# Kernel tuning notes

Measured on AMD Instinct MI355X. Metric: run time of the kernel, lower is better.

The kernel has to match this reference:

```python
import jax, jax.numpy as jnp
import numpy as np

D_MODEL = 768
N_LAYER = 4
VOCAB = 50257
D_STATE = 16
D_CONV = 4
D_INNER = 2 * D_MODEL
DT_RANK = 48
B, L = 1, 2048


def setup_inputs() -> dict:
    key = jax.random.key(0)
    ks = jax.random.split(key, 12)
    n = lambda k, shape, s=0.02: jax.random.normal(k, shape, dtype=jnp.float32) * s
    return {
        "idx": jax.random.randint(ks[0], (B, L), 0, VOCAB, dtype=jnp.int32),
        "targets": jax.random.randint(ks[1], (B, L), 0, VOCAB, dtype=jnp.int32),
        "embedding": n(ks[2], (VOCAB, D_MODEL)),
        "norm_w": jnp.ones((N_LAYER, D_MODEL), jnp.float32),
        "in_proj_w": n(ks[3], (N_LAYER, 2 * D_INNER, D_MODEL)),
        "conv_w": n(ks[4], (N_LAYER, D_INNER, D_CONV), 0.1),
        "conv_b": jnp.zeros((N_LAYER, D_INNER), jnp.float32),
        "x_proj_w": n(ks[5], (N_LAYER, DT_RANK + 2 * D_STATE, D_INNER)),
        "dt_proj_w": n(ks[6], (N_LAYER, D_INNER, DT_RANK), 0.1),
        # bias so softplus(dt) lands in ~[0.01, 0.1] as in the official init
        "dt_proj_b": jax.random.uniform(ks[7], (N_LAYER, D_INNER), jnp.float32, -4.6, -2.3),
        # A_log = log(1..d_state), the standard S4D-real init
        "A_log": jnp.log(jnp.broadcast_to(jnp.arange(1, D_STATE + 1, dtype=jnp.float32), (N_LAYER, D_INNER, D_STATE))),
        "D_param": jnp.ones((N_LAYER, D_INNER), jnp.float32),
        "out_proj_w": n(ks[8], (N_LAYER, D_MODEL, D_INNER)),
        "norm_f_w": jnp.ones((D_MODEL,), jnp.float32),
    }


def rmsnorm(x, w, eps=1e-5):
    return x * jax.lax.rsqrt(jnp.mean(x * x, -1, keepdims=True) + eps) * w


def causal_conv1d(x, w, b):
    # x: (B,L,d_inner); w: (d_inner, K) depthwise causal conv
    K = w.shape[-1]
    Lx = x.shape[1]
    xp = jnp.pad(x, ((0, 0), (K - 1, 0), (0, 0)))
    y = b
    for k in range(K):
        y = y + xp[:, k:k + Lx, :] * w[:, k]
    return y


def selective_scan(x, dt, A, Bm, Cm, Dp):
    # x, dt: (B,L,d_inner); A: (d_inner,d_state); Bm, Cm: (B,L,d_state)
    bsz, _, d_in = x.shape

    def step(h, inp):
        x_t, dt_t, B_t, C_t = inp  # (B,d_in),(B,d_in),(B,s),(B,s)
        h = jnp.exp(dt_t[:, :, None] * A) * h + (dt_t * x_t)[:, :, None] * B_t[:, None, :]
        return h, jnp.einsum('bds,bs->bd', h, C_t)

    h0 = jnp.zeros((bsz, d_in, A.shape[-1]), x.dtype)
    _, ys = jax.lax.scan(step, h0, (x.swapaxes(0, 1), dt.swapaxes(0, 1), Bm.swapaxes(0, 1), Cm.swapaxes(0, 1)))
    return ys.swapaxes(0, 1) + x * Dp


def mamba_block(x, in_w, cw, cb, xpw, dtw, dtb, a_log, dp, ow):
    xz = x @ in_w.T  # (B,L,2*d_inner)
    xi, z = jnp.split(xz, 2, axis=-1)
    xi = jax.nn.silu(causal_conv1d(xi, cw, cb))
    xdbl = xi @ xpw.T  # (B,L,dt_rank+2*d_state)
    dt = xdbl[..., :DT_RANK]
    Bm = xdbl[..., DT_RANK:DT_RANK + D_STATE]
    Cm = xdbl[..., DT_RANK + D_STATE:]
    dt = jax.nn.softplus(dt @ dtw.T + dtb)
    A = -jnp.exp(a_log)
    y = selective_scan(xi, dt, A, Bm, Cm, dp)
    y = y * jax.nn.silu(z)
    return y @ ow.T


def reference(idx, targets, embedding, norm_w, in_proj_w, conv_w, conv_b, x_proj_w,
              dt_proj_w, dt_proj_b, A_log, D_param, out_proj_w, norm_f_w):
    x = embedding[idx]  # (B,L,D)
    for l in range(N_LAYER):
        x = x + mamba_block(rmsnorm(x, norm_w[l]), in_proj_w[l], conv_w[l], conv_b[l],
                            x_proj_w[l], dt_proj_w[l], dt_proj_b[l], A_log[l],
                            D_param[l], out_proj_w[l])
    x = rmsnorm(x, norm_f_w)
    logits = x @ embedding.T  # tied lm head, (B,L,V)
    # cross_entropy with ignore_index=-1
    logp = jax.nn.log_softmax(logits, axis=-1)
    mask = (targets >= 0).astype(logits.dtype)
    tgt = jnp.clip(targets, 0, VOCAB - 1)
    nll = -jnp.take_along_axis(logp, tgt[..., None], axis=-1)[..., 0]
    loss = jnp.sum(nll * mask) / jnp.maximum(jnp.sum(mask), 1.0)
    return (logits, loss)
```

## Files before the change

### kernel.cpp

```cpp
#include <hip/hip_runtime.h>
#include <stdint.h>


#define D_MODEL 768
#define N_LAYER 4
#define VOCAB 50257
#define D_STATE 16
#define D_INNER 1536
#define DT_RANK 48
#define LSEQ 2048
#define TCHUNK 64
#define NCHUNK 32

#define EMB_E 39321600L
#define W1E 2359296L
#define W2E 196608L
#define W3E 98304L
#define W4E 1179648L
#define PERL (W1E + W2E + W3E + W4E)
#define TOTCVT (EMB_E + 4 * PERL)

typedef unsigned short u16;
typedef __attribute__((ext_vector_type(8))) short short8;
typedef __attribute__((ext_vector_type(4))) float f32x4;

__device__ __forceinline__ u16 f2bf(float f) {
  unsigned int x = __float_as_uint(f);
  x += 0x7fffu + ((x >> 16) & 1u);
  return (u16)(x >> 16);
}
__device__ __forceinline__ float bf2f(u16 v) {
  return __uint_as_float(((unsigned int)v) << 16);
}
__device__ __forceinline__ void gl16(const void* g, void* l) {
  __builtin_amdgcn_global_load_lds((const __attribute__((address_space(1))) void*)g,
                                   (__attribute__((address_space(3))) void*)l, 16, 0, 0);
}

__global__ void k_convert_all(const float* __restrict__ emb, const float* __restrict__ in_w,
                              const float* __restrict__ xp_w, const float* __restrict__ dt_w,
                              const float* __restrict__ out_w, u16* __restrict__ dst) {
  long i = (long)blockIdx.x * 256 + threadIdx.x;
  float v;
  if (i < EMB_E) {
    long n = i / D_MODEL, k = i % D_MODEL;
    v = (n < VOCAB) ? emb[n * D_MODEL + k] : 0.0f;
  } else {
    long j = i - EMB_E;
    int l = (int)(j / PERL);
    long m = j % PERL;
    if (m < W1E) {
      v = in_w[(long)l * W1E + m];
    } else if (m < W1E + W2E) {
      long mm = m - W1E;
      long n = mm / D_INNER, k = mm % D_INNER;
      v = (n < 80) ? xp_w[(long)l * 80 * D_INNER + n * D_INNER + k] : 0.0f;
    } else if (m < W1E + W2E + W3E) {
      long mm = m - (W1E + W2E);
      long n = mm / 64, k = mm % 64;
      v = (k < DT_RANK) ? dt_w[(long)l * D_INNER * DT_RANK + n * DT_RANK + k] : 0.0f;
    } else {
      long mm = m - (W1E + W2E + W3E);
      v = out_w[(long)l * W4E + mm];
    }
  }
  dst[i] = f2bf(v);
}

__global__ void k_embed_rms(const int* __restrict__ idx, const float* __restrict__ emb,
                            const float* __restrict__ w, float* __restrict__ x,
                            u16* __restrict__ xnb) {
  int t = blockIdx.x, tid = threadIdx.x;
  __shared__ float red[256];
  const float* src = emb + (long)idx[t] * D_MODEL;
  float g[3];
  float s = 0.0f;
#pragma unroll
  for (int q = 0; q < 3; q++) {
    g[q] = src[tid + q * 256];
    s += g[q] * g[q];
  }
  red[tid] = s; __syncthreads();
  for (int o = 128; o > 0; o >>= 1) { if (tid < o) red[tid] += red[tid + o]; __syncthreads(); }
  float scale = rsqrtf(red[0] / (float)D_MODEL + 1e-5f);
#pragma unroll
  for (int q = 0; q < 3; q++) {
    int c = tid + q * 256;
    x[(long)t * D_MODEL + c] = g[q];
    xnb[(long)t * D_MODEL + c] = f2bf(g[q] * scale * w[c]);
  }
}

__global__ void k_rms_red(const float* __restrict__ part, const float* __restrict__ w,
                          float* __restrict__ x, u16* __restrict__ xnb) {
  int t = blockIdx.x, tid = threadIdx.x;
  __shared__ float red[256];
  float g[3];
  float s = 0.0f;
#pragma unroll
  for (int q = 0; q < 3; q++) {
    int c = tid + q * 256;
    long off = (long)t * D_MODEL + c;
    float v = x[off];
#pragma unroll
    for (int p = 0; p < 4; p++) v += part[(size_t)p * LSEQ * D_MODEL + off];
    g[q] = v;
    s += v * v;
  }
  red[tid] = s; __syncthreads();
  for (int o = 128; o > 0; o >>= 1) { if (tid < o) red[tid] += red[tid + o]; __syncthreads(); }
  float scale = rsqrtf(red[0] / (float)D_MODEL + 1e-5f);
#pragma unroll
  for (int q = 0; q < 3; q++) {
    int c = tid + q * 256;
    x[(long)t * D_MODEL + c] = g[q];
    xnb[(long)t * D_MODEL + c] = f2bf(g[q] * scale * w[c]);
  }
}

template<int EPI>
__global__ __launch_bounds__(256) void k_gemm2(
    const u16* __restrict__ A, const u16* __restrict__ W, void* __restrict__ Cv,
    const float* __restrict__ bias, int N, int K, int lda, int ldb, int ldc) {
  __shared__ u16 lA[2][128 * 32];
  __shared__ u16 lB[2][128 * 32];
  const int gx = gridDim.x, gy = gridDim.y;
  int id = blockIdx.x + gx * blockIdx.y;
  int q8 = (gx * gy) >> 3;
  int v = (id & 7) * q8 + (id >> 3);
  const int bx = v / gy, by = v % gy;
  const int brow = by * 128, bcol = bx * 128;
  const int tid = threadIdx.x, wid = tid >> 6, lane = tid & 63;
  const int wm = (wid >> 1) * 64, wn = (wid & 1) * 64;
  const int fr = lane & 15, fq = lane >> 4, kh = fq * 8;
  const int srow = tid >> 2, scol = (tid & 3) * 8;
  const u16* ga0 = A + (size_t)(brow + srow) * lda + scol;
  const u16* ga1 = A + (size_t)(brow + srow + 64) * lda + scol;
  const u16* gb0 = W + (size_t)(bcol + srow) * ldb + scol;
  const u16* gb1 = W + (size_t)(bcol + srow + 64) * ldb + scol;
  const int lo = srow * 32 + scol;

  f32x4 acc[4][4];
#pragma unroll
  for (int i = 0; i < 4; i++)
#pragma unroll
    for (int j = 0; j < 4; j++)
#pragma unroll
      for (int r = 0; r < 4; r++) acc[i][j][r] = 0.0f;

  auto STAGE = [&](int k0, int b) {
    gl16(ga0 + k0, &lA[b][lo]);
    gl16(ga1 + k0, &lA[b][lo + 64 * 32]);
    gl16(gb0 + k0, &lB[b][lo]);
    gl16(gb1 + k0, &lB[b][lo + 64 * 32]);
  };

  const int nt = K / 32;
  STAGE(0, 0);
  __syncthreads();
  int cur = 0;
  for (int t = 0; t < nt; t++) {
    if (t + 1 < nt) STAGE((t + 1) * 32, cur ^ 1);
    short8 af[4], bfr[4];
#pragma unroll
    for (int i = 0; i < 4; i++) af[i] = *(const short8*)(&lA[cur][(wm + i * 16 + fr) * 32 + kh]);
#pragma unroll
    for (int j = 0; j < 4; j++) bfr[j] = *(const short8*)(&lB[cur][(wn + j * 16 + fr) * 32 + kh]);
#pragma unroll
    for (int i = 0; i < 4; i++)
#pragma unroll
      for (int j = 0; j < 4; j++)
        acc[i][j] = __builtin_amdgcn_mfma_f32_16x16x32_bf16(af[i], bfr[j], acc[i][j], 0, 0, 0);
    __syncthreads();
    cur ^= 1;
  }
#pragma unroll
  for (int i = 0; i < 4; i++)
#pragma unroll
    for (int j = 0; j < 4; j++) {
      int col = bcol + wn + j * 16 + fr;
      if (col < N) {
#pragma unroll
        for (int r = 0; r < 4; r++) {
          int row = brow + wm + i * 16 + fq * 4 + r;
          float val = acc[i][j][r];
          if (EPI == 1) {
            val += bias[col];
            val = (val > 20.0f) ? val : log1pf(__expf(val));
            ((float*)Cv)[(size_t)row * ldc + col] = val;
          } else {
            ((u16*)Cv)[(size_t)row * ldc + col] = f2bf(val);
          }
        }
      }
    }
}

__global__ __launch_bounds__(256) void k_gemm_part(
    const u16* __restrict__ A, const u16* __restrict__ W, float* __restrict__ Cp,
    int N, int Ks, int lda, int ldb, int ldc) {
  __shared__ u16 lA[2][128 * 32];
  __shared__ u16 lB[2][128 * 32];
  const int gx = gridDim.x, gy = gridDim.y;
  int id = blockIdx.x + gx * blockIdx.y;
  int q8 = (gx * gy) >> 3;
  int v = (id & 7) * q8 + (id >> 3);
  const int bx = v / gy, by = v % gy;
  const int brow = by * 128, bcol = bx * 128;
  const int koff = blockIdx.z * Ks;
  const int tid = threadIdx.x, wid = tid >> 6, lane = tid & 63;
  const int wm = (wid >> 1) * 64, wn = (wid & 1) * 64;
  const int fr = lane & 15, fq = lane >> 4, kh = fq * 8;
  const int srow = tid >> 2, scol = (tid & 3) * 8;
  const u16* ga0 = A + (size_t)(brow + srow) * lda + koff + scol;
  const u16* ga1 = A + (size_t)(brow + srow + 64) * lda + koff + scol;
  const u16* gb0 = W + (size_t)(bcol + srow) * ldb + koff + scol;
  const u16* gb1 = W + (size_t)(bcol + srow + 64) * ldb + koff + scol;
  const int lo = srow * 32 + scol;

  f32x4 acc[4][4];
#pragma unroll
  for (int i = 0; i < 4; i++)
#pragma unroll
    for (int j = 0; j < 4; j++)
#pragma unroll
      for (int r = 0; r < 4; r++) acc[i][j][r] = 0.0f;

  auto STAGE = [&](int k0, int b) {
    gl16(ga0 + k0, &lA[b][lo]);
    gl16(ga1 + k0, &lA[b][lo + 64 * 32]);
    gl16(gb0 + k0, &lB[b][lo]);
    gl16(gb1 + k0, &lB[b][lo + 64 * 32]);
  };

  const int nt = Ks / 32;
  STAGE(0, 0);
  __syncthreads();
  int cur = 0;
  for (int t = 0; t < nt; t++) {
    if (t + 1 < nt) STAGE((t + 1) * 32, cur ^ 1);
    short8 af[4], bfr[4];
#pragma unroll
    for (int i = 0; i < 4; i++) af[i] = *(const short8*)(&lA[cur][(wm + i * 16 + fr) * 32 + kh]);
#pragma unroll
    for (int j = 0; j < 4; j++) bfr[j] = *(const short8*)(&lB[cur][(wn + j * 16 + fr) * 32 + kh]);
#pragma unroll
    for (int i = 0; i < 4; i++)
#pragma unroll
      for (int j = 0; j < 4; j++)
        acc[i][j] = __builtin_amdgcn_mfma_f32_16x16x32_bf16(af[i], bfr[j], acc[i][j], 0, 0, 0);
    __syncthreads();
    cur ^= 1;
  }
  float* Cz = Cp + (size_t)blockIdx.z * LSEQ * ldc;
#pragma unroll
  for (int i = 0; i < 4; i++)
#pragma unroll
    for (int j = 0; j < 4; j++) {
      int col = bcol + wn + j * 16 + fr;
      if (col < N) {
#pragma unroll
        for (int r = 0; r < 4; r++) {
          int row = brow + wm + i * 16 + fq * 4 + r;
          Cz[(size_t)row * ldc + col] = acc[i][j][r];
        }
      }
    }
}

__global__ __launch_bounds__(256) void k_gemm_logits(
    const u16* __restrict__ A, const u16* __restrict__ W, float* __restrict__ C,
    float* __restrict__ part) {
  __shared__ u16 lA[2][128 * 32];
  __shared__ u16 lB[2][128 * 32];
  const int b = blockIdx.x;
  const int xcd = b & 7, slot = b >> 3;
  const int ct = xcd * 50 + (slot >> 4), rt = slot & 15;
  const int brow = rt * 128, bcol = ct * 128;
  const int tid = threadIdx.x, wid = tid >> 6, lane = tid & 63;
  const int wm = (wid >> 1) * 64, wn = (wid & 1) * 64;
  const int fr = lane & 15, fq = lane >> 4, kh = fq * 8;
  const int srow = tid >> 2, scol = (tid & 3) * 8;
  const u16* ga0 = A + (size_t)(brow + srow) * D_MODEL + scol;
  const u16* ga1 = A + (size_t)(brow + srow + 64) * D_MODEL + scol;
  const u16* gb0 = W + (size_t)(bcol + srow) * D_MODEL + scol;
  const u16* gb1 = W + (size_t)(bcol + srow + 64) * D_MODEL + scol;
  const int lo = srow * 32 + scol;

  f32x4 acc[4][4];
#pragma unroll
  for (int i = 0; i < 4; i++)
#pragma unroll
    for (int j = 0; j < 4; j++)
#pragma unroll
      for (int r = 0; r < 4; r++) acc[i][j][r] = 0.0f;

  auto STAGE = [&](int k0, int bb) {
    gl16(ga0 + k0, &lA[bb][lo]);
    gl16(ga1 + k0, &lA[bb][lo + 64 * 32]);
    gl16(gb0 + k0, &lB[bb][lo]);
    gl16(gb1 + k0, &lB[bb][lo + 64 * 32]);
  };

  STAGE(0, 0);
  __syncthreads();
  int cur = 0;
  for (int t = 0; t < D_MODEL / 32; t++) {
    if (t + 1 < D_MODEL / 32) STAGE((t + 1) * 32, cur ^ 1);
    short8 af[4], bfr[4];
#pragma unroll
    for (int i = 0; i < 4; i++) af[i] = *(const short8*)(&lA[cur][(wm + i * 16 + fr) * 32 + kh]);
#pragma unroll
    for (int j = 0; j < 4; j++) bfr[j] = *(const short8*)(&lB[cur][(wn + j * 16 + fr) * 32 + kh]);
#pragma unroll
    for (int i = 0; i < 4; i++)
#pragma unroll
      for (int j = 0; j < 4; j++)
        acc[i][j] = __builtin_amdgcn_mfma_f32_16x16x32_bf16(af[i], bfr[j], acc[i][j], 0, 0, 0);
    __syncthreads();
    cur ^= 1;
  }
  float rs[16];
#pragma unroll
  for (int q = 0; q < 16; q++) rs[q] = 0.0f;
#pragma unroll
  for (int i = 0; i < 4; i++)
#pragma unroll
    for (int j = 0; j < 4; j++) {
      int col = bcol + wn + j * 16 + fr;
      if (col < VOCAB) {
#pragma unroll
        for (int r = 0; r < 4; r++) {
          int row = brow + wm + i * 16 + fq * 4 + r;
          float val = acc[i][j][r];
          C[(size_t)row * VOCAB + col] = val;
          rs[i * 4 + r] += __expf(val - 20.0f);
        }
      }
    }
#pragma unroll
  for (int q = 0; q < 16; q++) {
    float s = rs[q];
    s += __shfl_xor(s, 1); s += __shfl_xor(s, 2);
    s += __shfl_xor(s, 4); s += __shfl_xor(s, 8);
    rs[q] = s;
  }
  if (fr == 0) {
    int pc = ct * 2 + (wn >> 6);
#pragma unroll
    for (int i = 0; i < 4; i++)
#pragma unroll
      for (int r = 0; r < 4; r++) {
        int row = brow + wm + i * 16 + fq * 4 + r;
        part[(size_t)pc * LSEQ + row] = rs[i * 4 + r];
      }
  }
}

__global__ void k_conv_silu(const u16* __restrict__ xzb, const float* __restrict__ cw,
                            const float* __restrict__ cb, u16* __restrict__ xib) {
  int i = blockIdx.x * 256 + threadIdx.x;
  int t = i / D_INNER, d = i % D_INNER;
  float acc = cb[d];
#pragma unroll
  for (int k = 0; k < 4; k++) {
    int tt = t - 3 + k;
    if (tt >= 0) acc += bf2f(xzb[(long)tt * (2 * D_INNER) + d]) * cw[d * 4 + k];
  }
  float s = acc / (1.0f + __expf(-acc));
  xib[i] = f2bf(s);
}

__global__ void k_red_xd(const float* __restrict__ pxp, float* __restrict__ xdbl,
                         u16* __restrict__ dtp) {
  int i = blockIdx.x * 256 + threadIdx.x;
  int t = i >> 7, k = i & 127;
  if (k < 80) {
    float s = 0.0f;
#pragma unroll
    for (int p = 0; p < 8; p++) s += pxp[(size_t)p * LSEQ * 80 + (long)t * 80 + k];
    xdbl[(long)t * 80 + k] = s;
    if (k < DT_RANK) dtp[(long)t * 64 + k] = f2bf(s);
    else if (k < 64) dtp[(long)t * 64 + k] = 0;
  }
}

__global__ void k_scanA(const float* __restrict__ dt, const u16* __restrict__ xi,
                        const float* __restrict__ xdbl, const float* __restrict__ a_log,
                        float* __restrict__ aprod, float* __restrict__ hend) {
  int d = blockIdx.x * 256 + threadIdx.x;
  int c = blockIdx.y;
  float A[16], ap[16], h[16];
#pragma unroll
  for (int s = 0; s < 16; s++) { A[s] = -__expf(a_log[d * 16 + s]); ap[s] = 1.0f; h[s] = 0.0f; }
  int t0 = c * TCHUNK;
  for (int t = t0; t < t0 + TCHUNK; t++) {
    float dtv = dt[(long)t * D_INNER + d], xv = bf2f(xi[(long)t * D_INNER + d]);
    float dx = dtv * xv;
    const float* Bp = xdbl + (long)t * 80 + DT_RANK;
#pragma unroll
    for (int s = 0; s < 16; s++) {
      float a = __expf(dtv * A[s]);
      h[s] = a * h[s] + dx * Bp[s];
      ap[s] *= a;
    }
  }
  long base = ((long)c * D_INNER + d) * 16;
#pragma unroll
  for (int s = 0; s < 16; s++) { aprod[base + s] = ap[s]; hend[base + s] = h[s]; }
}

__global__ void k_scanB(const float* __restrict__ aprod, const float* __restrict__ hend,
                        float* __restrict__ hinit) {
  int i = blockIdx.x * 256 + threadIdx.x;
  float h = 0.0f;
  for (int c = 0; c < NCHUNK; c++) {
    long idx = (long)c * D_INNER * 16 + i;
    hinit[idx] = h;
    h = aprod[idx] * h + hend[idx];
  }
}

__global__ void k_scanC(const float* __restrict__ dt, const u16* __restrict__ xi,
                        const float* __restrict__ xdbl, const float* __restrict__ a_log,
                        const float* __restrict__ hinit, const float* __restrict__ Dp,
                        const u16* __restrict__ xzb, u16* __restrict__ yb) {
  int d = blockIdx.x * 256 + threadIdx.x;
  int c = blockIdx.y;
  float A[16], h[16];
  long hb = (long)c * D_INNER * 16 + (long)d * 16;
#pragma unroll
  for (int s = 0; s < 16; s++) { A[s] = -__expf(a_log[d * 16 + s]); h[s] = hinit[hb + s]; }
  float Dv = Dp[d];
  int t0 = c * TCHUNK;
  for (int t = t0; t < t0 + TCHUNK; t++) {
    float dtv = dt[(long)t * D_INNER + d], xv = bf2f(xi[(long)t * D_INNER + d]);
    float dx = dtv * xv;
    const float* Bp = xdbl + (long)t * 80 + DT_RANK;
    const float* Cp = Bp + D_STATE;
    float o = xv * Dv;
#pragma unroll
    for (int s = 0; s < 16; s++) {
      float a = __expf(dtv * A[s]);
      h[s] = a * h[s] + dx * Bp[s];
      o += h[s] * Cp[s];
    }
    float z = bf2f(xzb[(long)t * (2 * D_INNER) + D_INNER + d]);
    yb[(long)t * D_INNER + d] = f2bf(o * (z / (1.0f + __expf(-z))));
  }
}

__global__ void k_lse_final(const float* __restrict__ part, const float* __restrict__ logits,
                            const int* __restrict__ tgt, float* __restrict__ nll,
                            float* __restrict__ msk) {
  int t = blockIdx.x * 256 + threadIdx.x;
  float s = 0.0f;
  for (int p = 0; p < 800; p++) s += part[(size_t)p * LSEQ + t];
  float lse = 20.0f + __logf(s);
  int tg = tgt[t];
  float mk = tg >= 0 ? 1.0f : 0.0f;
  int tc = tg < 0 ? 0 : (tg > VOCAB - 1 ? VOCAB - 1 : tg);
  nll[t] = (lse - logits[(size_t)t * VOCAB + tc]) * mk;
  msk[t] = mk;
}

__global__ void k_loss(const float* __restrict__ nll, const float* __restrict__ msk,
                       float* __restrict__ out) {
  int tid = threadIdx.x;
  __shared__ float r1[256], r2[256];
  float a = 0.0f, b = 0.0f;
  for (int i = tid; i < LSEQ; i += 256) { a += nll[i]; b += msk[i]; }
  r1[tid] = a; r2[tid] = b; __syncthreads();
  for (int o = 128; o > 0; o >>= 1) {
    if (tid < o) { r1[tid] += r1[tid + o]; r2[tid] += r2[tid + o]; }
    __syncthreads();
  }
  if (tid == 0) out[0] = r1[0] / fmaxf(r2[0], 1.0f);
}

extern "C" void kernel_launch(void* const* d_in, const int* in_sizes, int n_in,
                              void* d_out, int out_size, void* d_ws, size_t ws_size,
                              hipStream_t stream) {
  const int*   idx    = (const int*)d_in[0];
  const int*   tgt    = (const int*)d_in[1];
  const float* emb    = (const float*)d_in[2];
  const float* norm_w = (const float*)d_in[3];
  const float* in_w   = (const float*)d_in[4];
  const float* conv_w = (const float*)d_in[5];
  const float* conv_b = (const float*)d_in[6];
  const float* xp_w   = (const float*)d_in[7];
  const float* dt_w   = (const float*)d_in[8];
  const float* dt_b   = (const float*)d_in[9];
  const float* a_log  = (const float*)d_in[10];
  const float* d_par  = (const float*)d_in[11];
  const float* out_w  = (const float*)d_in[12];
  const float* normf  = (const float*)d_in[13];

  float* logits = (float*)d_out;
  float* loss   = logits + (size_t)LSEQ * VOCAB;

  char* base = (char*)d_ws;
  size_t off = 0;
  auto alloc = [&](size_t bytes) -> char* {
    char* r = base + off;
    off = (off + bytes + 255) & ~(size_t)255;
    return r;
  };
  u16*   wcat = (u16*)  alloc((size_t)TOTCVT * 2);
  float* x    = (float*)alloc((size_t)LSEQ * D_MODEL * 4);
  u16*   xnb  = (u16*)  alloc((size_t)LSEQ * D_MODEL * 2);
  u16*   xzb  = (u16*)  alloc((size_t)LSEQ * 2 * D_INNER * 2);
  u16*   xib  = (u16*)  alloc((size_t)LSEQ * D_INNER * 2);
  float* xdbl = (float*)alloc((size_t)LSEQ * 80 * 4);
  u16*   dtp  = (u16*)  alloc((size_t)LSEQ * 64 * 2);
  float* dtl  = (float*)alloc((size_t)LSEQ * D_INNER * 4);
  u16*   yb   = (u16*)  alloc((size_t)LSEQ * D_INNER * 2);
  float* pxp  = (float*)alloc((size_t)8 * LSEQ * 80 * 4);
  float* pop  = (float*)alloc((size_t)4 * LSEQ * D_MODEL * 4);
  float* apr  = (float*)alloc((size_t)NCHUNK * D_INNER * 16 * 4);
  float* hen  = (float*)alloc((size_t)NCHUNK * D_INNER * 16 * 4);
  float* hin  = (float*)alloc((size_t)NCHUNK * D_INNER * 16 * 4);
  float* nll  = (float*)alloc((size_t)LSEQ * 4);
  float* msk  = (float*)alloc((size_t)LSEQ * 4);
  float* part = pop;
  (void)ws_size; (void)in_sizes; (void)n_in; (void)out_size;

  const u16* embb = wcat;

  k_convert_all<<<(unsigned)(TOTCVT / 256), 256, 0, stream>>>(emb, in_w, xp_w, dt_w, out_w, wcat);
  k_embed_rms<<<LSEQ, 256, 0, stream>>>(idx, emb, norm_w, x, xnb);

  for (int l = 0; l < N_LAYER; l++) {
    const u16* w1 = wcat + EMB_E + (long)l * PERL;
    const u16* w2 = w1 + W1E;
    const u16* w3 = w2 + W2E;
    const u16* w4 = w3 + W3E;

    k_gemm2<2><<<dim3(24, 16), 256, 0, stream>>>(
        xnb, w1, xzb, nullptr, 2 * D_INNER, D_MODEL, D_MODEL, D_MODEL, 2 * D_INNER);

    k_conv_silu<<<(LSEQ * D_INNER) / 256, 256, 0, stream>>>(
        xzb, conv_w + (long)l * D_INNER * 4, conv_b + l * D_INNER, xib);

    k_gemm_part<<<dim3(1, 16, 8), 256, 0, stream>>>(
        xib, w2, pxp, 80, D_INNER / 8, D_INNER, D_INNER, 80);
    k_red_xd<<<(LSEQ * 128) / 256, 256, 0, stream>>>(pxp, xdbl, dtp);

    k_gemm2<1><<<dim3(12, 16), 256, 0, stream>>>(
        dtp, w3, dtl, dt_b + l * D_INNER, D_INNER, 64, 64, 64, D_INNER);

    const float* al = a_log + (long)l * D_INNER * D_STATE;
    k_scanA<<<dim3(D_INNER / 256, NCHUNK), 256, 0, stream>>>(dtl, xib, xdbl, al, apr, hen);
    k_scanB<<<(D_INNER * 16) / 256, 256, 0, stream>>>(apr, hen, hin);
    k_scanC<<<dim3(D_INNER / 256, NCHUNK), 256, 0, stream>>>(
        dtl, xib, xdbl, al, hin, d_par + l * D_INNER, xzb, yb);

    k_gemm_part<<<dim3(6, 16, 4), 256, 0, stream>>>(
        yb, w4, pop, D_MODEL, D_INNER / 4, D_INNER, D_INNER, D_MODEL);

    const float* wn = (l < N_LAYER - 1) ? (norm_w + (l + 1) * D_MODEL) : normf;
    k_rms_red<<<LSEQ, 256, 0, stream>>>(pop, wn, x, xnb);
  }

  k_gemm_logits<<<400 * 16, 256, 0, stream>>>(xnb, embb, logits, part);
  k_lse_final<<<LSEQ / 256, 256, 0, stream>>>(part, logits, tgt, nll, msk);
  k_loss<<<1, 256, 0, stream>>>(nll, msk, loss);
}
```

Measured before the change: 1.388 ms.

## Prefetch two K-tiles ahead in GEMMs with explicit waitcnt, vectorize conv_silu

The shared GEMM main loop is replaced by a macro that issues the first two tile loads up front, waits on vmcnt so one tile's loads stay in flight, and reissues loads into the buffer just consumed after a second barrier. This is meant to hide global-to-LDS latency better than the previous one-ahead loop with a full __syncthreads. Separately, the depthwise conv+SiLU kernel now processes 8 channels per thread with 16-byte vector loads and stores, cutting thread count and memory transactions. The hand-written waitcnt/barrier sequence depends on the exact count of outstanding loads and on the compiler not reordering around it.

```diff
diff --git a/kernel.cpp b/kernel.cpp
--- a/kernel.cpp
+++ b/kernel.cpp
@@ -36,6 +36,35 @@
   __builtin_amdgcn_global_load_lds((const __attribute__((address_space(1))) void*)g,
                                    (__attribute__((address_space(3))) void*)l, 16, 0, 0);
 }
+
+#define PIPELINE(NT)                                                          \
+  STAGE(0, 0);                                                                \
+  STAGE(32, 1);                                                               \
+  {                                                                           \
+    int cur = 0;                                                              \
+    for (int t = 0; t < (NT); t++) {                                          \
+      if (t + 1 < (NT)) { asm volatile("s_waitcnt vmcnt(4)" ::: "memory"); }  \
+      else              { asm volatile("s_waitcnt vmcnt(0)" ::: "memory"); }  \
+      asm volatile("s_barrier" ::: "memory");                                 \
+      short8 af[4], bfr[4];                                                   \
+      _Pragma("unroll")                                                       \
+      for (int i = 0; i < 4; i++)                                             \
+        af[i] = *(const short8*)(&lA[cur][(wm + i * 16 + fr) * 32 + kh]);     \
+      _Pragma("unroll")                                                       \
+      for (int j = 0; j < 4; j++)                                             \
+        bfr[j] = *(const short8*)(&lB[cur][(wn + j * 16 + fr) * 32 + kh]);    \
+      asm volatile("s_waitcnt lgkmcnt(0)" ::: "memory");                      \
+      asm volatile("s_barrier" ::: "memory");                                 \
+      if (t + 2 < (NT)) STAGE((t + 2) * 32, cur);                             \
+      _Pragma("unroll")                                                       \
+      for (int i = 0; i < 4; i++)                                             \
+        _Pragma("unroll")                                                     \
+        for (int j = 0; j < 4; j++)                                           \
+          acc[i][j] = __builtin_amdgcn_mfma_f32_16x16x32_bf16(af[i], bfr[j],  \
+                                                              acc[i][j], 0, 0, 0); \
+      cur ^= 1;                                                               \
+    }                                                                         \
+  }
 
 __global__ void k_convert_all(const float* __restrict__ emb, const float* __restrict__ in_w,
                               const float* __restrict__ xp_w, const float* __restrict__ dt_w,
@@ -150,30 +179,13 @@
 
   auto STAGE = [&](int k0, int b) {
     gl16(ga0 + k0, &lA[b][lo]);
-    gl16(ga1 + k0, &lA[b][lo + 64 * 32]);
+    gl16(ga1 + k0, &lA[b][lo + 2048]);
     gl16(gb0 + k0, &lB[b][lo]);
-    gl16(gb1 + k0, &lB[b][lo + 64 * 32]);
+    gl16(gb1 + k0, &lB[b][lo + 2048]);
   };
 
-  const int nt = K / 32;
-  STAGE(0, 0);
-  __syncthreads();
-  int cur = 0;
-  for (int t = 0; t < nt; t++) {
-    if (t + 1 < nt) STAGE((t + 1) * 32, cur ^ 1);
-    short8 af[4], bfr[4];
-#pragma unroll
-    for (int i = 0; i < 4; i++) af[i] = *(const short8*)(&lA[cur][(wm + i * 16 + fr) * 32 + kh]);
-#pragma unroll
-    for (int j = 0; j < 4; j++) bfr[j] = *(const short8*)(&lB[cur][(wn + j * 16 + fr) * 32 + kh]);
-#pragma unroll
-    for (int i = 0; i < 4; i++)
-#pragma unroll
-      for (int j = 0; j < 4; j++)
-        acc[i][j] = __builtin_amdgcn_mfma_f32_16x16x32_bf16(af[i], bfr[j], acc[i][j], 0, 0, 0);
-    __syncthreads();
-    cur ^= 1;
-  }
+  PIPELINE(K / 32);
+
 #pragma unroll
   for (int i = 0; i < 4; i++)
 #pragma unroll
@@ -228,30 +240,13 @@
 
   auto STAGE = [&](int k0, int b) {
     gl16(ga0 + k0, &lA[b][lo]);
-    gl16(ga1 + k0, &lA[b][lo + 64 * 32]);
+    gl16(ga1 + k0, &lA[b][lo + 2048]);
     gl16(gb0 + k0, &lB[b][lo]);
-    gl16(gb1 + k0, &lB[b][lo + 64 * 32]);
+    gl16(gb1 + k0, &lB[b][lo + 2048]);
   };
 
-  const int nt = Ks / 32;
-  STAGE(0, 0);
-  __syncthreads();
-  int cur = 0;
-  for (int t = 0; t < nt; t++) {
-    if (t + 1 < nt) STAGE((t + 1) * 32, cur ^ 1);
-    short8 af[4], bfr[4];
-#pragma unroll
-    for (int i = 0; i < 4; i++) af[i] = *(const short8*)(&lA[cur][(wm + i * 16 + fr) * 32 + kh]);
-#pragma unroll
-    for (int j = 0; j < 4; j++) bfr[j] = *(const short8*)(&lB[cur][(wn + j * 16 + fr) * 32 + kh]);
-#pragma unroll
-    for (int i = 0; i < 4; i++)
-#pragma unroll
-      for (int j = 0; j < 4; j++)
-        acc[i][j] = __builtin_amdgcn_mfma_f32_16x16x32_bf16(af[i], bfr[j], acc[i][j], 0, 0, 0);
-    __syncthreads();
-    cur ^= 1;
-  }
+  PIPELINE(Ks / 32);
+
   float* Cz = Cp + (size_t)blockIdx.z * LSEQ * ldc;
 #pragma unroll
   for (int i = 0; i < 4; i++)
@@ -297,29 +292,13 @@
 
   auto STAGE = [&](int k0, int bb) {
     gl16(ga0 + k0, &lA[bb][lo]);
-    gl16(ga1 + k0, &lA[bb][lo + 64 * 32]);
+    gl16(ga1 + k0, &lA[bb][lo + 2048]);
     gl16(gb0 + k0, &lB[bb][lo]);
-    gl16(gb1 + k0, &lB[bb][lo + 64 * 32]);
+    gl16(gb1 + k0, &lB[bb][lo + 2048]);
   };
 
-  STAGE(0, 0);
-  __syncthreads();
-  int cur = 0;
-  for (int t = 0; t < D_MODEL / 32; t++) {
-    if (t + 1 < D_MODEL / 32) STAGE((t + 1) * 32, cur ^ 1);
-    short8 af[4], bfr[4];
-#pragma unroll
-    for (int i = 0; i < 4; i++) af[i] = *(const short8*)(&lA[cur][(wm + i * 16 + fr) * 32 + kh]);
-#pragma unroll
-    for (int j = 0; j < 4; j++) bfr[j] = *(const short8*)(&lB[cur][(wn + j * 16 + fr) * 32 + kh]);
-#pragma unroll
-    for (int i = 0; i < 4; i++)
-#pragma unroll
-      for (int j = 0; j < 4; j++)
-        acc[i][j] = __builtin_amdgcn_mfma_f32_16x16x32_bf16(af[i], bfr[j], acc[i][j], 0, 0, 0);
-    __syncthreads();
-    cur ^= 1;
-  }
+  PIPELINE(D_MODEL / 32);
+
   float rs[16];
 #pragma unroll
   for (int q = 0; q < 16; q++) rs[q] = 0.0f;
@@ -360,15 +339,26 @@
 __global__ void k_conv_silu(const u16* __restrict__ xzb, const float* __restrict__ cw,
                             const float* __restrict__ cb, u16* __restrict__ xib) {
   int i = blockIdx.x * 256 + threadIdx.x;
-  int t = i / D_INNER, d = i % D_INNER;
-  float acc = cb[d];
+  int t = i / (D_INNER / 8), d8 = (i % (D_INNER / 8)) * 8;
+  float acc[8];
+#pragma unroll
+  for (int q = 0; q < 8; q++) acc[q] = cb[d8 + q];
 #pragma unroll
   for (int k = 0; k < 4; k++) {
     int tt = t - 3 + k;
-    if (tt >= 0) acc += bf2f(xzb[(long)tt * (2 * D_INNER) + d]) * cw[d * 4 + k];
-  }
-  float s = acc / (1.0f + __expf(-acc));
-  xib[i] = f2bf(s);
+    if (tt >= 0) {
+      short8 v = *(const short8*)(xzb + (long)tt * (2 * D_INNER) + d8);
+#pragma unroll
+      for (int q = 0; q < 8; q++) acc[q] += bf2f((u16)v[q]) * cw[(d8 + q) * 4 + k];
+    }
+  }
+  short8 o;
+#pragma unroll
+  for (int q = 0; q < 8; q++) {
+    float s = acc[q] / (1.0f + __expf(-acc[q]));
+    o[q] = (short)f2bf(s);
+  }
+  *(short8*)(xib + (long)t * D_INNER + d8) = o;
 }
 
 __global__ void k_red_xd(const float* __restrict__ pxp, float* __restrict__ xdbl,
@@ -539,7 +529,7 @@
     k_gemm2<2><<<dim3(24, 16), 256, 0, stream>>>(
         xnb, w1, xzb, nullptr, 2 * D_INNER, D_MODEL, D_MODEL, D_MODEL, 2 * D_INNER);
 
-    k_conv_silu<<<(LSEQ * D_INNER) / 256, 256, 0, stream>>>(
+    k_conv_silu<<<(LSEQ * D_INNER / 8) / 256, 256, 0, stream>>>(
         xzb, conv_w + (long)l * D_INNER * 4, conv_b + l * D_INNER, xib);
 
     k_gemm_part<<<dim3(1, 16, 8), 256, 0, stream>>>(
```

Result: faster. 1.210 ms (-12.8%).
